# Kernel tuning notes

Measured on AMD Instinct MI355X. Metric: run time of the kernel, lower is better.

Reference implementation:

```python
import jax, jax.numpy as jnp
import numpy as np

D_MODEL = 1024
N_HEADS = 16
HEAD_DIM = D_MODEL // N_HEADS


def setup_inputs() -> dict:
    key = jax.random.key(0)
    k1, k2, k3, k4, k5, k6 = jax.random.split(key, 6)
    B, T_q, T_kv = 4, 1024, 4096
    s = 1.0 / np.sqrt(D_MODEL)
    return {
        "query": jax.random.normal(k1, (B, T_q, D_MODEL), dtype=jnp.float32),
        "kv_source": jax.random.normal(k2, (B, T_kv, D_MODEL), dtype=jnp.float32),
        "w_q": jax.random.normal(k3, (D_MODEL, D_MODEL), dtype=jnp.float32) * s,
        "w_k": jax.random.normal(k4, (D_MODEL, D_MODEL), dtype=jnp.float32) * s,
        "w_v": jax.random.normal(k5, (D_MODEL, D_MODEL), dtype=jnp.float32) * s,
        "w_o": jax.random.normal(k6, (D_MODEL, D_MODEL), dtype=jnp.float32) * s,
    }


def reference(query, kv_source, w_q, w_k, w_v, w_o):
    B, T_q, _ = query.shape
    T_kv = kv_source.shape[1]
    # Linear(d,d,bias=False): y = x @ W^T
    q = (query @ w_q.T).reshape(B, T_q, N_HEADS, HEAD_DIM)
    k = (kv_source @ w_k.T).reshape(B, T_kv, N_HEADS, HEAD_DIM)
    v = (kv_source @ w_v.T).reshape(B, T_kv, N_HEADS, HEAD_DIM)
    scale = HEAD_DIM ** -0.5
    # scores: (B, H, T_q, T_kv)
    attn = jax.nn.softmax(jnp.einsum('bqhd,bkhd->bhqk', q, k) * scale, axis=-1)
    out = jnp.einsum('bhqk,bkhd->bqhd', attn, v).reshape(B, T_q, D_MODEL)
    return out @ w_o.T
```

## Files before the change

kernel.cpp:

```cpp
#include <hip/hip_runtime.h>
#include <hip/hip_bf16.h>


typedef __attribute__((ext_vector_type(4))) float f32x4;
typedef __attribute__((ext_vector_type(8))) short bf16x8;

__device__ __forceinline__ unsigned short f2bf(float f) {
  unsigned u = __float_as_uint(f);
  u = (u + 0x7fffu + ((u >> 16) & 1u)) >> 16;
  return (unsigned short)u;
}

#define GLD_LDS16(g, l)                                                     \
  __builtin_amdgcn_global_load_lds(                                        \
      (const __attribute__((address_space(1))) unsigned int*)(const void*)(g), \
      (__attribute__((address_space(3))) unsigned int*)(void*)(l), 16, 0, 0)

__global__ void cvt_all(const float* __restrict__ q, const float* __restrict__ kv,
                        const float* __restrict__ wq, const float* __restrict__ wk,
                        const float* __restrict__ wv, const float* __restrict__ wo,
                        unsigned short* __restrict__ q_bf,
                        unsigned short* __restrict__ kv_bf,
                        unsigned short* __restrict__ wq_bf,
                        unsigned short* __restrict__ wk_bf,
                        unsigned short* __restrict__ wv_bf,
                        unsigned short* __restrict__ wo_bf) {
  const int QN = 4194304, KVN = 16777216, WN = 1048576;
  const float SC = 0.125f * 1.44269504088896f;
  int total_quads = (QN + KVN + 4 * WN) >> 2;
  int stride = gridDim.x * blockDim.x;
  for (int t = blockIdx.x * blockDim.x + threadIdx.x; t < total_quads; t += stride) {
    int i = t << 2;
    const float* src;
    unsigned short* dst;
    float sc = 1.0f;
    int off;
    if (i < QN) { src = q; dst = q_bf; off = i; }
    else if (i < QN + KVN) { src = kv; dst = kv_bf; off = i - QN; }
    else if (i < QN + KVN + WN) { src = wq; dst = wq_bf; off = i - QN - KVN; sc = SC; }
    else if (i < QN + KVN + 2 * WN) { src = wk; dst = wk_bf; off = i - QN - KVN - WN; }
    else if (i < QN + KVN + 3 * WN) { src = wv; dst = wv_bf; off = i - QN - KVN - 2 * WN; }
    else { src = wo; dst = wo_bf; off = i - QN - KVN - 3 * WN; }
    float4 v = *(const float4*)(src + off);
    ushort4 r;
    r.x = f2bf(v.x * sc); r.y = f2bf(v.y * sc);
    r.z = f2bf(v.z * sc); r.w = f2bf(v.w * sc);
    *(ushort4*)(dst + off) = r;
  }
}

template <int WRITE_BF16>
__global__ __launch_bounds__(256) void gemm_bt(
    const unsigned short* __restrict__ A, const unsigned short* __restrict__ Bt,
    void* __restrict__ Cp, int M, int N, int K, int ldc) {
  __shared__ __align__(16) unsigned short Ash[4096];
  __shared__ __align__(16) unsigned short Bsh[4096];

  int tiles_n = N >> 7;
  int nwg = gridDim.x;
  int wg = blockIdx.x;
  int cpx = nwg >> 3;
  wg = (wg & 7) * cpx + (wg >> 3);
  int tm = wg / tiles_n, tn = wg - tm * tiles_n;

  int tid = threadIdx.x;
  int lane = tid & 63, wave = tid >> 6;
  int wr = wave >> 1, wc = wave & 1;
  int brow = tm << 7, bcol = tn << 7;

  int fr = lane & 15, fg = lane >> 4;
  int swz = (fr >> 1) & 3;

  int srow = lane >> 2;
  int sg = (lane & 3) ^ ((srow >> 1) & 3);

  const unsigned short* aG0 = A + (size_t)(brow + wave * 32 + srow) * K + sg * 8;
  const unsigned short* aG1 = A + (size_t)(brow + wave * 32 + 16 + srow) * K + sg * 8;
  const unsigned short* bG0 = Bt + (size_t)(bcol + wave * 32 + srow) * K + sg * 8;
  const unsigned short* bG1 = Bt + (size_t)(bcol + wave * 32 + 16 + srow) * K + sg * 8;
  unsigned short* aL0 = Ash + wave * 1024;
  unsigned short* aL1 = Ash + wave * 1024 + 512;
  unsigned short* bL0 = Bsh + wave * 1024;
  unsigned short* bL1 = Bsh + wave * 1024 + 512;

  const f32x4 zero4 = {0.f, 0.f, 0.f, 0.f};
  f32x4 acc[4][4];
#pragma unroll
  for (int m = 0; m < 4; ++m)
#pragma unroll
    for (int n = 0; n < 4; ++n) acc[m][n] = zero4;

  for (int k0 = 0; k0 < K; k0 += 32) {
    GLD_LDS16(aG0 + k0, aL0);
    GLD_LDS16(aG1 + k0, aL1);
    GLD_LDS16(bG0 + k0, bL0);
    GLD_LDS16(bG1 + k0, bL1);
    __syncthreads();

    bf16x8 af[4], bfr[4];
#pragma unroll
    for (int m = 0; m < 4; ++m) {
      int r = wr * 64 + m * 16 + fr;
      af[m] = *(const bf16x8*)(Ash + r * 32 + ((fg ^ swz) * 8));
    }
#pragma unroll
    for (int n = 0; n < 4; ++n) {
      int r = wc * 64 + n * 16 + fr;
      bfr[n] = *(const bf16x8*)(Bsh + r * 32 + ((fg ^ swz) * 8));
    }
#pragma unroll
    for (int m = 0; m < 4; ++m)
#pragma unroll
      for (int n = 0; n < 4; ++n)
        acc[m][n] =
            __builtin_amdgcn_mfma_f32_16x16x32_bf16(af[m], bfr[n], acc[m][n], 0, 0, 0);
    __syncthreads();
  }

  int crow = brow + wr * 64 + fg * 4;
  int ccol = bcol + wc * 64 + fr;
#pragma unroll
  for (int m = 0; m < 4; ++m)
#pragma unroll
    for (int n = 0; n < 4; ++n)
#pragma unroll
      for (int j = 0; j < 4; ++j) {
        size_t off = (size_t)(crow + m * 16 + j) * ldc + (ccol + n * 16);
        if (WRITE_BF16)
          ((unsigned short*)Cp)[off] = f2bf(acc[m][n][j]);
        else
          ((float*)Cp)[off] = acc[m][n][j];
      }
}

__global__ __launch_bounds__(512) void attn_fwd(
    const unsigned short* __restrict__ qp,
    const unsigned short* __restrict__ kp,
    const unsigned short* __restrict__ vt,
    unsigned short* __restrict__ ao) {
  __shared__ __align__(16) unsigned short Ksh[128 * 64];
  __shared__ __align__(16) unsigned short Vsh[64 * 128];
  __shared__ __align__(16) unsigned short Psh[8][16 * 72];

  int idx = (blockIdx.x & 7) * 64 + (blockIdx.x >> 3);
  int qt = idx & 7;
  int h = (idx >> 3) & 15;
  int b = idx >> 7;
  int tid = threadIdx.x;
  int lane = tid & 63, w = tid >> 6;
  int fr = lane & 15, fg = lane >> 4;

  int qrow = b * 1024 + qt * 128 + w * 16 + fr;
  bf16x8 qf0 = *(const bf16x8*)(qp + (size_t)qrow * 1024 + h * 64 + fg * 8);
  bf16x8 qf1 = *(const bf16x8*)(qp + (size_t)qrow * 1024 + h * 64 + 32 + fg * 8);

  bf16x8 ones;
#pragma unroll
  for (int e = 0; e < 8; ++e) ones[e] = (short)0x3F80;

  const f32x4 zero4 = {0.f, 0.f, 0.f, 0.f};
  f32x4 o[4];
#pragma unroll
  for (int n = 0; n < 4; ++n) o[n] = zero4;
  float m[4], ssum[4];
#pragma unroll
  for (int j = 0; j < 4; ++j) { m[j] = -1e30f; ssum[j] = 0.f; }

  int rK = w * 16 + (lane >> 3);
  int gK = (lane & 7) ^ ((lane >> 3) & 7);
  const unsigned short* ksrc = kp + (size_t)(b * 4096 + rK) * 1024 + h * 64 + gK * 8;
  int dV = w * 8 + (lane >> 4);
  int gV = (lane & 15) ^ (dV & 15);
  int gV1 = (lane & 15) ^ ((dV + 4) & 15);
  const unsigned short* vsrc0 = vt + (size_t)(h * 64 + dV) * 16384 + b * 4096 + gV * 8;
  const unsigned short* vsrc1 =
      vt + (size_t)(h * 64 + dV + 4) * 16384 + b * 4096 + gV1 * 8;

  unsigned short* pw = &Psh[w][0];

  for (int kv0 = 0; kv0 < 4096; kv0 += 128) {
    GLD_LDS16(ksrc + (size_t)kv0 * 1024, Ksh + w * 1024);
    GLD_LDS16(ksrc + (size_t)kv0 * 1024 + 8192, Ksh + w * 1024 + 512);
    GLD_LDS16(vsrc0 + kv0, Vsh + w * 1024);
    GLD_LDS16(vsrc1 + kv0, Vsh + w * 1024 + 512);
    __syncthreads();

    f32x4 S[8];
#pragma unroll
    for (int s = 0; s < 8; ++s) S[s] = zero4;
    __builtin_amdgcn_s_setprio(1);
#pragma unroll
    for (int s = 0; s < 8; ++s) {
      const unsigned short* krow = Ksh + (s * 16 + fr) * 64;
      bf16x8 kf0 = *(const bf16x8*)(krow + ((fg ^ (fr & 7)) * 8));
      bf16x8 kf1 = *(const bf16x8*)(krow + (((4 + fg) ^ (fr & 7)) * 8));
      S[s] = __builtin_amdgcn_mfma_f32_16x16x32_bf16(qf0, kf0, S[s], 0, 0, 0);
      S[s] = __builtin_amdgcn_mfma_f32_16x16x32_bf16(qf1, kf1, S[s], 0, 0, 0);
    }
    __builtin_amdgcn_s_setprio(0);

    float cm[4];
#pragma unroll
    for (int j = 0; j < 4; ++j) cm[j] = S[0][j];
#pragma unroll
    for (int s = 1; s < 8; ++s)
#pragma unroll
      for (int j = 0; j < 4; ++j) cm[j] = fmaxf(cm[j], S[s][j]);
#pragma unroll
    for (int mask = 1; mask <= 8; mask <<= 1)
#pragma unroll
      for (int j = 0; j < 4; ++j) cm[j] = fmaxf(cm[j], __shfl_xor(cm[j], mask));

    bool grow = (cm[0] > m[0]) | (cm[1] > m[1]) | (cm[2] > m[2]) | (cm[3] > m[3]);
    if (__any(grow)) {
#pragma unroll
      for (int j = 0; j < 4; ++j) {
        float mn = fmaxf(m[j], cm[j]);
        float fsc = exp2f(m[j] - mn);
        m[j] = mn;
        ssum[j] *= fsc;
#pragma unroll
        for (int n = 0; n < 4; ++n) o[n][j] *= fsc;
      }
    }

    f32x4 rsum = zero4;
#pragma unroll
    for (int hf = 0; hf < 2; ++hf) {
#pragma unroll
      for (int sp = 0; sp < 4; sp += 2) {
        int s = hf * 4 + sp;
#pragma unroll
        for (int j = 0; j < 4; ++j) {
          float p0 = exp2f(S[s][j] - m[j]);
          float p1 = exp2f(S[s + 1][j] - m[j]);
          __hip_bfloat162 pk = __float22bfloat162_rn(float2{p0, p1});
          unsigned u = *reinterpret_cast<unsigned*>(&pk);
          int base = (fg * 4 + j) * 72 + sp * 16 + fr;
          pw[base] = (unsigned short)u;
          pw[base + 16] = (unsigned short)(u >> 16);
        }
      }
      __builtin_amdgcn_s_setprio(1);
#pragma unroll
      for (int kk = 0; kk < 2; ++kk) {
        bf16x8 pa = *(const bf16x8*)(pw + fr * 72 + (kk * 4 + fg) * 8);
        rsum = __builtin_amdgcn_mfma_f32_16x16x32_bf16(pa, ones, rsum, 0, 0, 0);
        int g = hf * 8 + kk * 4 + fg;
#pragma unroll
        for (int n = 0; n < 4; ++n) {
          bf16x8 vf = *(const bf16x8*)(Vsh + (n * 16 + fr) * 128 + ((g ^ fr) * 8));
          o[n] = __builtin_amdgcn_mfma_f32_16x16x32_bf16(pa, vf, o[n], 0, 0, 0);
        }
      }
      __builtin_amdgcn_s_setprio(0);
    }
#pragma unroll
    for (int j = 0; j < 4; ++j) ssum[j] += rsum[j];
    __syncthreads();
  }

#pragma unroll
  for (int j = 0; j < 4; ++j) {
    float inv = 1.0f / ssum[j];
    int row = b * 1024 + qt * 128 + w * 16 + fg * 4 + j;
#pragma unroll
    for (int n = 0; n < 4; ++n)
      ao[(size_t)row * 1024 + h * 64 + n * 16 + fr] = f2bf(o[n][j] * inv);
  }
}

extern "C" void kernel_launch(void* const* d_in, const int* in_sizes, int n_in,
                              void* d_out, int out_size, void* d_ws, size_t ws_size,
                              hipStream_t stream) {
  const float* query = (const float*)d_in[0];
  const float* kvs = (const float*)d_in[1];
  const float* wq = (const float*)d_in[2];
  const float* wk = (const float*)d_in[3];
  const float* wv = (const float*)d_in[4];
  const float* wo = (const float*)d_in[5];
  float* out = (float*)d_out;
  char* ws = (char*)d_ws;
  const size_t MB = 1ull << 20;

  unsigned short* q_bf = (unsigned short*)(ws + 0 * MB);
  unsigned short* kv_bf = (unsigned short*)(ws + 8 * MB);
  unsigned short* wq_bf = (unsigned short*)(ws + 40 * MB);
  unsigned short* wk_bf = (unsigned short*)(ws + 42 * MB);
  unsigned short* wv_bf = (unsigned short*)(ws + 44 * MB);
  unsigned short* wo_bf = (unsigned short*)(ws + 46 * MB);
  unsigned short* qp = (unsigned short*)(ws + 48 * MB);
  unsigned short* kp = (unsigned short*)(ws + 56 * MB);
  unsigned short* vt = (unsigned short*)(ws + 88 * MB);
  unsigned short* ao = (unsigned short*)(ws + 120 * MB);

  cvt_all<<<2048, 256, 0, stream>>>(query, kvs, wq, wk, wv, wo, q_bf, kv_bf,
                                    wq_bf, wk_bf, wv_bf, wo_bf);

  gemm_bt<1><<<256, 256, 0, stream>>>(q_bf, wq_bf, qp, 4096, 1024, 1024, 1024);
  gemm_bt<1><<<1024, 256, 0, stream>>>(kv_bf, wk_bf, kp, 16384, 1024, 1024, 1024);
  gemm_bt<1><<<1024, 256, 0, stream>>>(wv_bf, kv_bf, vt, 1024, 16384, 1024, 16384);

  attn_fwd<<<512, 512, 0, stream>>>(qp, kp, vt, ao);

  gemm_bt<0><<<256, 256, 0, stream>>>(ao, wo_bf, out, 4096, 1024, 1024, 1024);
}
```

Baseline: 440.6 us.

## Rewrite attention with 32x32 MFMA transposed scores and register-resident P

The attention kernel now computes S^T with 32x32x16 bf16 MFMAs, so each lane owns one query row. That makes the row max mostly in-register with a single cross-half shuffle. P is repacked into MFMA operand layout with v_permlane32_swap instead of going through LDS, which removes the Psh buffer and its LDS round trip. Blocks shrink to 2 waves covering 64 query rows, with 1024 blocks and new K/V swizzles. The cost is more global->LDS loads per wave and possibly lower K/V reuse per block.

```diff
diff --git a/kernel.cpp b/kernel.cpp
--- a/kernel.cpp
+++ b/kernel.cpp
@@ -3,12 +3,17 @@
 
 
 typedef __attribute__((ext_vector_type(4))) float f32x4;
+typedef __attribute__((ext_vector_type(16))) float f32x16;
 typedef __attribute__((ext_vector_type(8))) short bf16x8;
 
 __device__ __forceinline__ unsigned short f2bf(float f) {
   unsigned u = __float_as_uint(f);
   u = (u + 0x7fffu + ((u >> 16) & 1u)) >> 16;
   return (unsigned short)u;
+}
+
+__device__ __forceinline__ void pl32swap(unsigned& x, unsigned& y) {
+  asm volatile("v_permlane32_swap_b32 %0, %1" : "+v"(x), "+v"(y));
 }
 
 #define GLD_LDS16(g, l)                                                     \
@@ -133,141 +138,157 @@
       }
 }
 
-__global__ __launch_bounds__(512) void attn_fwd(
+__global__ __launch_bounds__(128) void attn_fwd(
     const unsigned short* __restrict__ qp,
     const unsigned short* __restrict__ kp,
     const unsigned short* __restrict__ vt,
     unsigned short* __restrict__ ao) {
   __shared__ __align__(16) unsigned short Ksh[128 * 64];
   __shared__ __align__(16) unsigned short Vsh[64 * 128];
-  __shared__ __align__(16) unsigned short Psh[8][16 * 72];
-
-  int idx = (blockIdx.x & 7) * 64 + (blockIdx.x >> 3);
-  int qt = idx & 7;
-  int h = (idx >> 3) & 15;
-  int b = idx >> 7;
+
+  int idx = (blockIdx.x & 7) * 128 + (blockIdx.x >> 3);
+  int qt = idx & 15;
+  int h = (idx >> 4) & 15;
+  int b = idx >> 8;
   int tid = threadIdx.x;
   int lane = tid & 63, w = tid >> 6;
-  int fr = lane & 15, fg = lane >> 4;
-
-  int qrow = b * 1024 + qt * 128 + w * 16 + fr;
-  bf16x8 qf0 = *(const bf16x8*)(qp + (size_t)qrow * 1024 + h * 64 + fg * 8);
-  bf16x8 qf1 = *(const bf16x8*)(qp + (size_t)qrow * 1024 + h * 64 + 32 + fg * 8);
+  int q5 = lane & 31, hi = lane >> 5;
+
+  const unsigned short* qptr =
+      qp + (size_t)(b * 1024 + qt * 64 + w * 32 + q5) * 1024 + h * 64 + hi * 8;
+  bf16x8 qf[4];
+#pragma unroll
+  for (int s = 0; s < 4; ++s) qf[s] = *(const bf16x8*)(qptr + s * 16);
 
   bf16x8 ones;
 #pragma unroll
   for (int e = 0; e < 8; ++e) ones[e] = (short)0x3F80;
 
-  const f32x4 zero4 = {0.f, 0.f, 0.f, 0.f};
-  f32x4 o[4];
-#pragma unroll
-  for (int n = 0; n < 4; ++n) o[n] = zero4;
-  float m[4], ssum[4];
-#pragma unroll
-  for (int j = 0; j < 4; ++j) { m[j] = -1e30f; ssum[j] = 0.f; }
-
-  int rK = w * 16 + (lane >> 3);
-  int gK = (lane & 7) ^ ((lane >> 3) & 7);
-  const unsigned short* ksrc = kp + (size_t)(b * 4096 + rK) * 1024 + h * 64 + gK * 8;
-  int dV = w * 8 + (lane >> 4);
-  int gV = (lane & 15) ^ (dV & 15);
-  int gV1 = (lane & 15) ^ ((dV + 4) & 15);
-  const unsigned short* vsrc0 = vt + (size_t)(h * 64 + dV) * 16384 + b * 4096 + gV * 8;
-  const unsigned short* vsrc1 =
-      vt + (size_t)(h * 64 + dV + 4) * 16384 + b * 4096 + gV1 * 8;
-
-  unsigned short* pw = &Psh[w][0];
-
-  for (int kv0 = 0; kv0 < 4096; kv0 += 128) {
-    GLD_LDS16(ksrc + (size_t)kv0 * 1024, Ksh + w * 1024);
-    GLD_LDS16(ksrc + (size_t)kv0 * 1024 + 8192, Ksh + w * 1024 + 512);
-    GLD_LDS16(vsrc0 + kv0, Vsh + w * 1024);
-    GLD_LDS16(vsrc1 + kv0, Vsh + w * 1024 + 512);
+  f32x16 O[2], rsum;
+#pragma unroll
+  for (int r = 0; r < 16; ++r) { O[0][r] = 0.f; O[1][r] = 0.f; rsum[r] = 0.f; }
+  float mrun = -1e30f;
+
+  const unsigned short* kS[8];
+#pragma unroll
+  for (int i = 0; i < 8; ++i) {
+    int row = w * 64 + i * 8 + (lane >> 3);
+    int g = (lane & 7) ^ ((row ^ (2 * (row >> 3))) & 7);
+    kS[i] = kp + (size_t)(b * 4096 + row) * 1024 + h * 64 + g * 8;
+  }
+  const unsigned short* vS[8];
+#pragma unroll
+  for (int i = 0; i < 8; ++i) {
+    int row = w * 32 + i * 4 + (lane >> 4);
+    int g = (lane & 15) ^ ((row >> 1) & 14);
+    vS[i] = vt + (size_t)(h * 64 + row) * 16384 + b * 4096 + g * 8;
+  }
+
+  int xk = hi ^ ((q5 ^ (2 * (q5 >> 3))) & 7);
+  int koff[4];
+#pragma unroll
+  for (int s = 0; s < 4; ++s) koff[s] = q5 * 64 + (((2 * s) ^ xk) * 8);
+  int xv = hi ^ ((q5 >> 1) & 14);
+  int voff[4][2];
+#pragma unroll
+  for (int kt = 0; kt < 4; ++kt)
+#pragma unroll
+    for (int p = 0; p < 2; ++p)
+      voff[kt][p] = q5 * 128 + (((4 * kt + 2 * p) ^ xv) * 8);
+
+  for (int it = 0; it < 32; ++it) {
+#pragma unroll
+    for (int i = 0; i < 8; ++i) GLD_LDS16(kS[i], Ksh + w * 4096 + i * 512);
+#pragma unroll
+    for (int i = 0; i < 8; ++i) GLD_LDS16(vS[i], Vsh + w * 4096 + i * 512);
+#pragma unroll
+    for (int i = 0; i < 8; ++i) { kS[i] += 131072; vS[i] += 128; }
     __syncthreads();
 
-    f32x4 S[8];
-#pragma unroll
-    for (int s = 0; s < 8; ++s) S[s] = zero4;
+    f32x16 S[4];
+#pragma unroll
+    for (int kt = 0; kt < 4; ++kt)
+#pragma unroll
+      for (int r = 0; r < 16; ++r) S[kt][r] = 0.f;
     __builtin_amdgcn_s_setprio(1);
 #pragma unroll
-    for (int s = 0; s < 8; ++s) {
-      const unsigned short* krow = Ksh + (s * 16 + fr) * 64;
-      bf16x8 kf0 = *(const bf16x8*)(krow + ((fg ^ (fr & 7)) * 8));
-      bf16x8 kf1 = *(const bf16x8*)(krow + (((4 + fg) ^ (fr & 7)) * 8));
-      S[s] = __builtin_amdgcn_mfma_f32_16x16x32_bf16(qf0, kf0, S[s], 0, 0, 0);
-      S[s] = __builtin_amdgcn_mfma_f32_16x16x32_bf16(qf1, kf1, S[s], 0, 0, 0);
-    }
+    for (int kt = 0; kt < 4; ++kt)
+#pragma unroll
+      for (int s = 0; s < 4; ++s) {
+        bf16x8 kf = *(const bf16x8*)(Ksh + kt * 2048 + koff[s]);
+        S[kt] = __builtin_amdgcn_mfma_f32_32x32x16_bf16(kf, qf[s], S[kt], 0, 0, 0);
+      }
     __builtin_amdgcn_s_setprio(0);
 
-    float cm[4];
-#pragma unroll
-    for (int j = 0; j < 4; ++j) cm[j] = S[0][j];
-#pragma unroll
-    for (int s = 1; s < 8; ++s)
-#pragma unroll
-      for (int j = 0; j < 4; ++j) cm[j] = fmaxf(cm[j], S[s][j]);
-#pragma unroll
-    for (int mask = 1; mask <= 8; mask <<= 1)
-#pragma unroll
-      for (int j = 0; j < 4; ++j) cm[j] = fmaxf(cm[j], __shfl_xor(cm[j], mask));
-
-    bool grow = (cm[0] > m[0]) | (cm[1] > m[1]) | (cm[2] > m[2]) | (cm[3] > m[3]);
-    if (__any(grow)) {
-#pragma unroll
-      for (int j = 0; j < 4; ++j) {
-        float mn = fmaxf(m[j], cm[j]);
-        float fsc = exp2f(m[j] - mn);
-        m[j] = mn;
-        ssum[j] *= fsc;
-#pragma unroll
-        for (int n = 0; n < 4; ++n) o[n][j] *= fsc;
-      }
-    }
-
-    f32x4 rsum = zero4;
-#pragma unroll
-    for (int hf = 0; hf < 2; ++hf) {
-#pragma unroll
-      for (int sp = 0; sp < 4; sp += 2) {
-        int s = hf * 4 + sp;
-#pragma unroll
-        for (int j = 0; j < 4; ++j) {
-          float p0 = exp2f(S[s][j] - m[j]);
-          float p1 = exp2f(S[s + 1][j] - m[j]);
-          __hip_bfloat162 pk = __float22bfloat162_rn(float2{p0, p1});
-          unsigned u = *reinterpret_cast<unsigned*>(&pk);
-          int base = (fg * 4 + j) * 72 + sp * 16 + fr;
-          pw[base] = (unsigned short)u;
-          pw[base + 16] = (unsigned short)(u >> 16);
-        }
-      }
+    float t[16];
+#pragma unroll
+    for (int r = 0; r < 16; ++r)
+      t[r] = fmaxf(fmaxf(S[0][r], S[1][r]), fmaxf(S[2][r], S[3][r]));
+#pragma unroll
+    for (int st = 8; st >= 1; st >>= 1)
+#pragma unroll
+      for (int r = 0; r < 8; ++r)
+        if (r < st) t[r] = fmaxf(t[r], t[r + st]);
+    float cmax = fmaxf(t[0], __shfl_xor(t[0], 32));
+
+    if (__any(cmax > mrun)) {
+      float mn = fmaxf(mrun, cmax);
+      float fsc = exp2f(mrun - mn);
+      mrun = mn;
+#pragma unroll
+      for (int r = 0; r < 16; ++r) {
+        rsum[r] *= fsc; O[0][r] *= fsc; O[1][r] *= fsc;
+      }
+    }
+
+#pragma unroll
+    for (int kt = 0; kt < 4; ++kt) {
+      float p[16];
+#pragma unroll
+      for (int r = 0; r < 16; ++r) p[r] = exp2f(S[kt][r] - mrun);
+      unsigned u[8];
+#pragma unroll
+      for (int i = 0; i < 8; ++i) {
+        __hip_bfloat162 pk = __float22bfloat162_rn(float2{p[2 * i], p[2 * i + 1]});
+        u[i] = *reinterpret_cast<unsigned*>(&pk);
+      }
+      pl32swap(u[0], u[2]);
+      pl32swap(u[1], u[3]);
+      pl32swap(u[4], u[6]);
+      pl32swap(u[5], u[7]);
+      union PU { unsigned uu[4]; bf16x8 v; };
+      PU a0; a0.uu[0] = u[0]; a0.uu[1] = u[1]; a0.uu[2] = u[2]; a0.uu[3] = u[3];
+      PU a1; a1.uu[0] = u[4]; a1.uu[1] = u[5]; a1.uu[2] = u[6]; a1.uu[3] = u[7];
+      bf16x8 pf0 = a0.v, pf1 = a1.v;
+
       __builtin_amdgcn_s_setprio(1);
-#pragma unroll
-      for (int kk = 0; kk < 2; ++kk) {
-        bf16x8 pa = *(const bf16x8*)(pw + fr * 72 + (kk * 4 + fg) * 8);
-        rsum = __builtin_amdgcn_mfma_f32_16x16x32_bf16(pa, ones, rsum, 0, 0, 0);
-        int g = hf * 8 + kk * 4 + fg;
-#pragma unroll
-        for (int n = 0; n < 4; ++n) {
-          bf16x8 vf = *(const bf16x8*)(Vsh + (n * 16 + fr) * 128 + ((g ^ fr) * 8));
-          o[n] = __builtin_amdgcn_mfma_f32_16x16x32_bf16(pa, vf, o[n], 0, 0, 0);
-        }
+      rsum = __builtin_amdgcn_mfma_f32_32x32x16_bf16(ones, pf0, rsum, 0, 0, 0);
+      rsum = __builtin_amdgcn_mfma_f32_32x32x16_bf16(ones, pf1, rsum, 0, 0, 0);
+#pragma unroll
+      for (int dt = 0; dt < 2; ++dt) {
+        bf16x8 vf0 = *(const bf16x8*)(Vsh + voff[kt][0] + dt * 4096);
+        bf16x8 vf1 = *(const bf16x8*)(Vsh + voff[kt][1] + dt * 4096);
+        O[dt] = __builtin_amdgcn_mfma_f32_32x32x16_bf16(vf0, pf0, O[dt], 0, 0, 0);
+        O[dt] = __builtin_amdgcn_mfma_f32_32x32x16_bf16(vf1, pf1, O[dt], 0, 0, 0);
       }
       __builtin_amdgcn_s_setprio(0);
     }
-#pragma unroll
-    for (int j = 0; j < 4; ++j) ssum[j] += rsum[j];
     __syncthreads();
   }
 
-#pragma unroll
-  for (int j = 0; j < 4; ++j) {
-    float inv = 1.0f / ssum[j];
-    int row = b * 1024 + qt * 128 + w * 16 + fg * 4 + j;
-#pragma unroll
-    for (int n = 0; n < 4; ++n)
-      ao[(size_t)row * 1024 + h * 64 + n * 16 + fr] = f2bf(o[n][j] * inv);
-  }
+  float inv = 1.0f / rsum[0];
+  size_t obase = (size_t)(b * 1024 + qt * 64 + w * 32 + q5) * 1024 + h * 64;
+#pragma unroll
+  for (int dt = 0; dt < 2; ++dt)
+#pragma unroll
+    for (int j2 = 0; j2 < 4; ++j2) {
+      ushort4 pk;
+      pk.x = f2bf(O[dt][4 * j2 + 0] * inv);
+      pk.y = f2bf(O[dt][4 * j2 + 1] * inv);
+      pk.z = f2bf(O[dt][4 * j2 + 2] * inv);
+      pk.w = f2bf(O[dt][4 * j2 + 3] * inv);
+      *(ushort4*)(ao + obase + dt * 32 + j2 * 8 + hi * 4) = pk;
+    }
 }
 
 extern "C" void kernel_launch(void* const* d_in, const int* in_sizes, int n_in,
@@ -301,7 +322,7 @@
   gemm_bt<1><<<1024, 256, 0, stream>>>(kv_bf, wk_bf, kp, 16384, 1024, 1024, 1024);
   gemm_bt<1><<<1024, 256, 0, stream>>>(wv_bf, kv_bf, vt, 1024, 16384, 1024, 16384);
 
-  attn_fwd<<<512, 512, 0, stream>>>(qp, kp, vt, ao);
+  attn_fwd<<<1024, 128, 0, stream>>>(qp, kp, vt, ao);
 
   gemm_bt<0><<<256, 256, 0, stream>>>(ao, wo_bf, out, 4096, 1024, 1024, 1024);
 }
```

New measurement: 500.6 us. 1.14x slower.
